# Optimization experiments

Hardware: AMD Instinct MI355X
Metric: run time of the kernel (lower is better)

Reference implementation:

```python
import jax, jax.numpy as jnp
import numpy as np

B, S, V, E, HL = 64, 30, 5000, 300, 256
TWOH = 2 * HL
KB, MAPD, MEMD, MLP, NCLS = 512, 512, 512, 1024, 32
L, T, NMOD, NOPS = 8, 9, 9, 6
IH, IW, CIN = 15, 10, 512 + 128


def setup_inputs():
    key = jax.random.key(0)
    ks = iter(jax.random.split(key, 64))
    g = lambda shape, s=0.05: jax.random.normal(next(ks), shape, jnp.float32) * s
    inp = {}
    inp['image'] = g((B, CIN, IH, IW), 1.0)
    inp['ques'] = jax.random.randint(next(ks), (B, S), 0, V)
    ql = jnp.sort(jax.random.randint(next(ks), (B,), 1, S + 1))[::-1]
    inp['q_len'] = ql.at[0].set(S)
    inp['embed_W'] = g((V, E))
    for d in ('f', 'b'):
        inp['lstm_Wi_' + d] = g((E, 4 * HL))
        inp['lstm_Wh_' + d] = g((HL, 4 * HL))
        inp['lstm_b_' + d] = jnp.zeros((4 * HL,), jnp.float32)
    inp['W1'] = g((T, TWOH, TWOH))
    inp['b_1'] = jnp.zeros((TWOH,), jnp.float32)
    inp['W2_w'] = g((2 * TWOH, TWOH)); inp['W2_b'] = jnp.zeros((TWOH,), jnp.float32)
    inp['W3'] = g((TWOH,))
    inp['c_0'] = g((TWOH,), 1.0)
    inp['Wmod'] = g((TWOH, NMOD))
    inp['ic1_w'] = g((KB, CIN)); inp['ic1_b'] = g((KB,), 1.0)
    inp['ic2_w'] = g((KB, KB)); inp['ic2_b'] = g((KB,), 1.0)
    inp['i2m_w'] = g((MAPD, KB)); inp['i2m_b'] = g((MAPD,), 1.0)
    inp['t2m_w'] = g((TWOH, MAPD)); inp['t2m_b'] = jnp.zeros((MAPD,), jnp.float32)
    inp['cell3_ow'] = g((4, NOPS), 1.0)
    inp['cell3_cw'] = g((4, MAPD)); inp['cell3_cb'] = jnp.zeros((4,), jnp.float32)
    inp['cell4_ow'] = g((2, NOPS), 1.0)
    inp['cell4_cw'] = g((2, MAPD)); inp['cell4_cb'] = jnp.zeros((2,), jnp.float32)
    inp['ans_ow'] = g((2, NOPS), 1.0)
    inp['ans_W'] = g((2, 2 * MAPD, MEMD)); inp['ans_b'] = jnp.zeros((2, MEMD), jnp.float32)
    inp['out1_w'] = g((TWOH + MEMD, MLP)); inp['out1_b'] = jnp.zeros((MLP,), jnp.float32)
    inp['out2_w'] = g((MLP, NCLS)); inp['out2_b'] = jnp.zeros((NCLS,), jnp.float32)
    return inp


def _conv1x1(x, w, b):
    return jnp.einsum('bchw,oc->bohw', x, w) + b[None, :, None, None]


def _lstm_dir(xW, Wh, mask, reverse):
    # xW: [S,B,4H], mask: [S,B,1] ; torch LSTM gate order i,f,g,o
    Bn, Hn = xW.shape[1], Wh.shape[0]
    def step(carry, inp):
        h, c = carry
        xw, m = inp
        z = xw + h @ Wh
        i, f, gg, o = jnp.split(z, 4, axis=-1)
        cn = jax.nn.sigmoid(f) * c + jax.nn.sigmoid(i) * jnp.tanh(gg)
        hn = jax.nn.sigmoid(o) * jnp.tanh(cn)
        return (jnp.where(m, hn, h), jnp.where(m, cn, c)), jnp.where(m, hn, 0.0)
    init = (jnp.zeros((Bn, Hn), xW.dtype), jnp.zeros((Bn, Hn), xW.dtype))
    (hF, _), outs = jax.lax.scan(step, init, (xW, mask), reverse=reverse)
    return hF, outs


def _mix3(ow, x, a, t):
    # soft op mixing (DARTS-style) for 3-input cells: x [B,D,H,W], a [B,H,W], t [B,D]
    w = jax.nn.softmax(ow)
    a4 = a[:, None]; t4 = t[:, :, None, None]
    ops = (x * t4, x + t4, x * a4, x * t4 * a4, x, a4 * t4)
    return jax.nn.elu(sum(w[k] * ops[k] for k in range(NOPS)))


def _mix4(ow, x, a1, a2, t):
    w = jax.nn.softmax(ow)
    a14 = a1[:, None]; a24 = a2[:, None]; t4 = t[:, :, None, None]
    ops = (x * t4, x + t4, x * a14, x * a24, x * a14 * a24, x * t4 * (a14 + a24))
    return jax.nn.elu(sum(w[k] * ops[k] for k in range(NOPS)))


def _forward(image, ques, q_len, embed_W, lstm_Wi_f, lstm_Wh_f, lstm_b_f, lstm_Wi_b, lstm_Wh_b, lstm_b_b, W1, b_1, W2_w, W2_b, W3, c_0, Wmod, ic1_w, ic1_b, ic2_w, ic2_b, i2m_w, i2m_b, t2m_w, t2m_b, cell3_ow, cell3_cw, cell3_cb, cell4_ow, cell4_cw, cell4_cb, ans_ow, ans_W, ans_b, out1_w, out1_b, out2_w, out2_b):
    # img_conv (1x1 conv -> ELU -> 1x1 conv)
    x = jax.nn.elu(_conv1x1(image, ic1_w, ic1_b))
    x = _conv1x1(x, ic2_w, ic2_b)
    Bn, _, Hh, Ww = x.shape
    Sn = ques.shape[1]
    # bi-LSTM over the (packed, i.e. masked) question
    emb = embed_W[ques]                                   # [B,S,E]
    mask = (jnp.arange(Sn)[None, :] < q_len[:, None])     # [B,S]
    mT = mask.T[:, :, None].astype(x.dtype) > 0           # [S,B,1] bool
    xWf = (emb @ lstm_Wi_f + lstm_b_f).transpose(1, 0, 2)
    xWb = (emb @ lstm_Wi_b + lstm_b_b).transpose(1, 0, 2)
    hF, oF = _lstm_dir(xWf, lstm_Wh_f, mT, False)
    hB, oB = _lstm_dir(xWb, lstm_Wh_b, mT, True)
    lstm_out = jnp.concatenate([oF, oB], -1).transpose(1, 0, 2)  # [B,S,2H], zero at pads
    q = jnp.concatenate([hF, hB], -1)                            # [B,2H]
    img_map = _conv1x1(x, i2m_w, i2m_b)                          # [B,MAP,H,W]
    stack = jnp.zeros((Bn, Hh, Ww, L), x.dtype)
    p = jnp.zeros((Bn, L), x.dtype).at[:, 0].set(1.0)
    mem = jnp.zeros((Bn, MEMD), x.dtype)
    c_prev = jnp.tile(c_0[None], (Bn, 1))
    e0 = jnp.zeros((L,), x.dtype).at[0].set(1.0)
    imp_loss = jnp.float32(0.0)
    read = lambda st, pp: jnp.einsum('bhwl,bl->bhw', st, pp)
    dec = lambda pp: jnp.concatenate([pp[:, 1:], jnp.zeros_like(pp[:, :1])], 1) + pp * e0
    for t in range(T):
        u = jnp.concatenate([q @ W1[t] + b_1, c_prev], 1) @ W2_w + W2_b  # [B,2H]
        wl = u @ Wmod                                                     # [B,9]
        ls = jax.nn.log_softmax(wl, axis=1)
        imp_loss = imp_loss - jnp.sum(jnp.exp(ls) * ls)
        w = jnp.exp(ls)
        attn = jax.nn.softmax(jnp.einsum('bsh,h->bs', lstm_out * u[:, None, :], W3), axis=1)
        c = jnp.einsum('bs,bsh->bh', attn, lstm_out)
        c_prev = c
        tmap = c @ t2m_w + t2m_b
        stacks, ps = [], []
        a_top = read(stack, p)     # attention at stack top
        # modules 0-3: overwrite at current pointer (pointer shift is commented out in source)
        for m in range(4):
            out = jnp.einsum('bdhw,d->bhw', _mix3(cell3_ow[m], img_map, a_top, tmap), cell3_cw[m]) + cell3_cb[m]
            pb = p[:, None, None, :]
            stacks.append(stack * (1.0 - pb) + out[..., None] * pb)
            ps.append(p)
        # modules 4-5: pop one (soft pointer decrement), then write
        p_dec = dec(p)
        a2 = read(stack, p_dec)
        for m in range(2):
            out = jnp.einsum('bdhw,d->bhw', _mix4(cell4_ow[m], img_map, a_top, a2, tmap), cell4_cw[m]) + cell4_cb[m]
            pb = p_dec[:, None, None, :]
            stacks.append(stack * (1.0 - pb) + out[..., None] * pb)
            ps.append(p_dec)
        # modules 6-7: answer cells -> memory update, stack untouched
        pooled6 = jnp.mean(_mix3(ans_ow[0], img_map, a_top, tmap), axis=(2, 3))
        mem6 = jnp.concatenate([pooled6, tmap], 1) @ ans_W[0] + ans_b[0]
        stacks.append(stack); ps.append(p)
        pooled7 = jnp.mean(_mix4(ans_ow[1], img_map, a_top, a2, tmap), axis=(2, 3))
        mem7 = jnp.concatenate([pooled7, tmap], 1) @ ans_W[1] + ans_b[1]
        stacks.append(stack); ps.append(p_dec)
        # module 8: NoOp
        stacks.append(stack); ps.append(p)
        # soft mixing over modules (the scatter-heavy part)
        stack = jnp.einsum('bm,bmhwl->bhwl', w, jnp.stack(stacks, 1))
        p = jnp.einsum('bm,bml->bl', w, jnp.stack(ps, 1))
        mem = w[:, 6:7] * mem6 + w[:, 7:8] * mem7 + (1.0 - w[:, 6:7] - w[:, 7:8]) * mem
    h1 = jax.nn.elu(jnp.concatenate([q, mem], 1) @ out1_w + out1_b)
    logits = h1 @ out2_w + out2_b
    return logits, imp_loss


def reference(image, ques, q_len, embed_W, lstm_Wi_f, lstm_Wh_f, lstm_b_f, lstm_Wi_b, lstm_Wh_b, lstm_b_b, W1, b_1, W2_w, W2_b, W3, c_0, Wmod, ic1_w, ic1_b, ic2_w, ic2_b, i2m_w, i2m_b, t2m_w, t2m_b, cell3_ow, cell3_cw, cell3_cb, cell4_ow, cell4_cw, cell4_cb, ans_ow, ans_W, ans_b, out1_w, out1_b, out2_w, out2_b):
    return _forward(image, ques, q_len, embed_W, lstm_Wi_f, lstm_Wh_f, lstm_b_f, lstm_Wi_b, lstm_Wh_b, lstm_b_b, W1, b_1, W2_w, W2_b, W3, c_0, Wmod, ic1_w, ic1_b, ic2_w, ic2_b, i2m_w, i2m_b, t2m_w, t2m_b, cell3_ow, cell3_cw, cell3_cb, cell4_ow, cell4_cw, cell4_cb, ans_ow, ans_W, ans_b, out1_w, out1_b, out2_w, out2_b)
```

## Files before the change

### kernel.cpp

```cpp
#include <hip/hip_runtime.h>
#include <math.h>

#define DEV __device__ __forceinline__

DEV float fexp(float x){ return __expf(x); }
DEV float elu_(float x){ return x > 0.f ? x : fexp(x) - 1.f; }
DEV float sigm_(float x){ return 1.f/(1.f + fexp(-x)); }
DEV float tanh_(float x){ float e = fexp(2.f*x); return 1.f - 2.f/(e + 1.f); }
DEV unsigned bf16r(float x){ unsigned u = __float_as_uint(x);
  return (u + 0x7fffu + ((u>>16)&1u)) >> 16; }
DEV float blo(unsigned u){ return __uint_as_float(u << 16); }
DEV float bhi(unsigned u){ return __uint_as_float(u & 0xffff0000u); }
DEV float bl(unsigned short u){ return __uint_as_float(((unsigned)u) << 16); }

using frag  = __attribute__((ext_vector_type(8))) short;
using f32x4 = __attribute__((ext_vector_type(4))) float;

DEV void d_pack4(const float* __restrict__ Whf, const float* __restrict__ Whb,
                 uint4* __restrict__ whp4, int idx)
{
  int dir = idx >> 15;
  int rem = idx & 32767;
  int kg  = rem >> 10;
  int n   = rem & 1023;
  const float* Wh = dir ? Whb : Whf;
  unsigned v[4];
#pragma unroll
  for (int j = 0; j < 4; ++j) {
    int k = kg*8 + 2*j;
    float lo = Wh[(size_t)k*1024 + n];
    float hi = Wh[(size_t)(k+1)*1024 + n];
    v[j] = bf16r(lo) | (bf16r(hi) << 16);
  }
  whp4[idx] = make_uint4(v[0], v[1], v[2], v[3]);
}

DEV void d_packB(const float* __restrict__ W, short* __restrict__ Bp,
                 int KC, int Ng, int Ksrc, int N, int trans, int idx)
{
  if (idx >= KC*Ng*64) return;
  int lane = idx & 63;
  int g    = (idx >> 6) % Ng;
  int kc   = idx / (64*Ng);
  int n = g*16 + (lane & 15);
  int kb = kc*32 + ((lane >> 4) << 3);
  unsigned o[4];
#pragma unroll
  for (int jj = 0; jj < 4; ++jj) {
    int k0 = kb + 2*jj;
    float v0 = (k0   < Ksrc) ? (trans ? W[(size_t)n*Ksrc + k0]   : W[(size_t)(k0)*N + n])   : 0.f;
    float v1 = (k0+1 < Ksrc) ? (trans ? W[(size_t)n*Ksrc + k0+1] : W[(size_t)(k0+1)*N + n]) : 0.f;
    o[jj] = bf16r(v0) | (bf16r(v1) << 16);
  }
  *(uint4*)(Bp + (size_t)idx*8) = make_uint4(o[0], o[1], o[2], o[3]);
}

DEV void d_packImg(const float* __restrict__ image, short* __restrict__ Ap, int idx)
{
  int lane = idx & 63;
  int kc   = (idx >> 6) % 20;
  int mt   = idx / 1280;
  int row = mt*16 + (lane & 15);
  int b = row / 150, p = row % 150;
  int cb = kc*32 + ((lane >> 4) << 3);
  unsigned o[4];
#pragma unroll
  for (int jj = 0; jj < 4; ++jj) {
    float v0 = image[((size_t)b*640 + cb + 2*jj    )*150 + p];
    float v1 = image[((size_t)b*640 + cb + 2*jj + 1)*150 + p];
    o[jj] = bf16r(v0) | (bf16r(v1) << 16);
  }
  *(uint4*)(Ap + (size_t)idx*8) = make_uint4(o[0], o[1], o[2], o[3]);
}

DEV void d_packEmb(const float* __restrict__ embedW, const int* __restrict__ ques,
                   short* __restrict__ Ap, int idx)
{
  int lane = idx & 63;
  int kc   = (idx >> 6) % 10;
  int mt   = idx / 640;
  int row = mt*16 + (lane & 15);
  int q = ques[row];
  int kb = kc*32 + ((lane >> 4) << 3);
  unsigned o[4];
#pragma unroll
  for (int jj = 0; jj < 4; ++jj) {
    int k0 = kb + 2*jj;
    float v0 = (k0   < 300) ? embedW[(size_t)q*300 + k0]   : 0.f;
    float v1 = (k0+1 < 300) ? embedW[(size_t)q*300 + k0+1] : 0.f;
    o[jj] = bf16r(v0) | (bf16r(v1) << 16);
  }
  *(uint4*)(Ap + (size_t)idx*8) = make_uint4(o[0], o[1], o[2], o[3]);
}

__global__ __launch_bounds__(256)
void megapack_k(const float* __restrict__ c0, const float* __restrict__ c3ow,
                const float* __restrict__ c4ow, const float* __restrict__ aow,
                float* __restrict__ stack, float* __restrict__ pvecA,
                float* __restrict__ mem, float* __restrict__ cprev,
                float* __restrict__ swb, float* __restrict__ pl,
                const float* __restrict__ Whf, const float* __restrict__ Whb,
                uint4* __restrict__ whp4,
                const float* __restrict__ ic1w, short* __restrict__ w1p,
                const float* __restrict__ ic2w, short* __restrict__ w2mp,
                const float* __restrict__ i2mw, short* __restrict__ w3mp,
                const float* __restrict__ Wif, short* __restrict__ wifp,
                const float* __restrict__ Wib, short* __restrict__ wibp,
                const float* __restrict__ image, short* __restrict__ imgP,
                const float* __restrict__ embedW, const int* __restrict__ ques,
                short* __restrict__ embp,
                const float* __restrict__ t2mw, unsigned* __restrict__ t2pp,
                const float* __restrict__ W2w, unsigned short* __restrict__ w2bp,
                const float* __restrict__ ansW, unsigned short* __restrict__ answp)
{
  const int bx = blockIdx.x, tid = threadIdx.x;
  if (bx < 320) {
    int idx = bx*256 + tid;
    int stride = 320*256;
    for (int i = idx; i < 64*150*8; i += stride) stack[i] = 0.f;
    for (int i = idx; i < 64*8;    i += stride) pvecA[i] = ((i & 7) == 0) ? 1.f : 0.f;
    for (int i = idx; i < 64*512;  i += stride) mem[i] = 0.f;
    for (int i = idx; i < 64*512;  i += stride) cprev[i] = c0[i & 511];
    for (int i = idx; i < 9*2*64*512; i += stride) pl[i] = 0.f;
    if (idx < 8) {
      const float* ow = (idx < 4) ? (c3ow + idx*6)
                      : (idx < 6) ? (c4ow + (idx-4)*6)
                                  : (aow  + (idx-6)*6);
      float mx = ow[0];
      for (int m = 1; m < 6; ++m) mx = fmaxf(mx, ow[m]);
      float e[6]; float s = 0.f;
      for (int m = 0; m < 6; ++m) { e[m] = fexp(ow[m]-mx); s += e[m]; }
      for (int m = 0; m < 6; ++m) swb[idx*6+m] = e[m]/s;
    }
  } else if (bx < 576) {
    d_pack4(Whf, Whb, whp4, (bx-320)*256 + tid);
  } else if (bx < 736) {
    d_packB(ic1w, w1p, 20, 32, 640, 512, 1, (bx-576)*256 + tid);
  } else if (bx < 864) {
    d_packB(ic2w, w2mp, 16, 32, 512, 512, 1, (bx-736)*256 + tid);
  } else if (bx < 992) {
    d_packB(i2mw, w3mp, 16, 32, 512, 512, 1, (bx-864)*256 + tid);
  } else if (bx < 1152) {
    d_packB(Wif, wifp, 10, 64, 300, 1024, 0, (bx-992)*256 + tid);
  } else if (bx < 1312) {
    d_packB(Wib, wibp, 10, 64, 300, 1024, 0, (bx-1152)*256 + tid);
  } else if (bx < 4312) {
    d_packImg(image, imgP, (bx-1312)*256 + tid);
  } else if (bx < 4612) {
    d_packEmb(embedW, ques, embp, (bx-4312)*256 + tid);
  } else if (bx < 5124) {
    int idx = (bx-4612)*256 + tid;
    int k = idx >> 8, c = idx & 255;
    t2pp[idx] = bf16r(t2mw[(size_t)k*512 + c]) | (bf16r(t2mw[(size_t)k*512 + 256 + c]) << 16);
  } else if (bx < 7172) {
    int i = (bx-5124)*256 + tid;
    w2bp[i] = (unsigned short)bf16r(W2w[i]);
  } else {
    int i = (bx-7172)*256 + tid;
    answp[i] = (unsigned short)bf16r(ansW[i]);
  }
}

__global__ __launch_bounds__(256)
void gemmM_k(const short* __restrict__ ApA, const short* __restrict__ ApB,
             const short* __restrict__ BpA, const short* __restrict__ BpB,
             const float* __restrict__ biasA, const float* __restrict__ biasB,
             void* __restrict__ CoutA, void* __restrict__ CoutB,
             int KC, int Ng, int N, int mode, int act, int KCout)
{
  __shared__ float lds[4][16][68];
  const int z = blockIdx.z;
  const short* Ap = z ? ApB : ApA;
  const short* Bp = z ? BpB : BpA;
  const float* bias = z ? biasB : biasA;
  void* Cout = z ? CoutB : CoutA;
  const int tid = threadIdx.x, lane = tid & 63, w = tid >> 6;
  const int mt = blockIdx.y*4 + w;
  const int ncol0 = blockIdx.x*64;
  const short* Abase = Ap + (((size_t)mt*KC) << 9) + lane*8;
  const short* Bbase = Bp + (((size_t)blockIdx.x*4) << 9) + lane*8;
  f32x4 acc0 = {0.f,0.f,0.f,0.f}, acc1 = acc0, acc2 = acc0, acc3 = acc0;
#pragma unroll 2
  for (int kc = 0; kc < KC; ++kc) {
    frag a = *(const frag*)(Abase + ((size_t)kc << 9));
    const short* bk = Bbase + (((size_t)kc*Ng) << 9);
    frag b0 = *(const frag*)(bk);
    frag b1 = *(const frag*)(bk + 512);
    frag b2 = *(const frag*)(bk + 1024);
    frag b3 = *(const frag*)(bk + 1536);
    acc0 = __builtin_amdgcn_mfma_f32_16x16x32_bf16(a, b0, acc0, 0, 0, 0);
    acc1 = __builtin_amdgcn_mfma_f32_16x16x32_bf16(a, b1, acc1, 0, 0, 0);
    acc2 = __builtin_amdgcn_mfma_f32_16x16x32_bf16(a, b2, acc2, 0, 0, 0);
    acc3 = __builtin_amdgcn_mfma_f32_16x16x32_bf16(a, b3, acc3, 0, 0, 0);
  }
  {
    int colb = lane & 15, rowb = (lane >> 4)*4;
#pragma unroll
    for (int r = 0; r < 4; ++r) {
      lds[w][rowb+r][ 0+colb] = acc0[r];
      lds[w][rowb+r][16+colb] = acc1[r];
      lds[w][rowb+r][32+colb] = acc2[r];
      lds[w][rowb+r][48+colb] = acc3[r];
    }
  }
  __syncthreads();
  if (mode == 0) {
    float* C = (float*)Cout;
    int mloc = lane >> 2, q4 = lane & 3;
    size_t rowoff = (size_t)(mt*16 + mloc)*N + ncol0 + q4*16;
#pragma unroll
    for (int i = 0; i < 4; ++i) {
      float4 v = *(float4*)&lds[w][mloc][q4*16 + i*4];
      const float* bp = bias + ncol0 + q4*16 + i*4;
      v.x += bp[0]; v.y += bp[1]; v.z += bp[2]; v.w += bp[3];
      if (act) { v.x = elu_(v.x); v.y = elu_(v.y); v.z = elu_(v.z); v.w = elu_(v.w); }
      *(float4*)&C[rowoff + i*4] = v;
    }
  } else if (mode == 1) {
    short* C = (short*)Cout;
    int m = lane & 15, qb = (lane >> 4)*8;
#pragma unroll
    for (int h = 0; h < 2; ++h) {
      int nl = h*32 + qb;
      unsigned o[4];
#pragma unroll
      for (int jj = 0; jj < 4; ++jj) {
        float v0 = lds[w][m][nl + 2*jj]     + bias[ncol0 + nl + 2*jj];
        float v1 = lds[w][m][nl + 2*jj + 1] + bias[ncol0 + nl + 2*jj + 1];
        if (act) { v0 = elu_(v0); v1 = elu_(v1); }
        o[jj] = bf16r(v0) | (bf16r(v1) << 16);
      }
      *(uint4*)(C + (((size_t)mt*KCout + (ncol0 >> 5) + h) << 9) + lane*8)
          = make_uint4(o[0], o[1], o[2], o[3]);
    }
  } else {
    unsigned short* C = (unsigned short*)Cout;
    int row = lane >> 2, cb = (lane & 3)*16;
#pragma unroll
    for (int h = 0; h < 2; ++h) {
      unsigned o[4];
#pragma unroll
      for (int jj = 0; jj < 4; ++jj) {
        float v0 = lds[w][row][cb + h*8 + 2*jj]     + bias[ncol0 + cb + h*8 + 2*jj];
        float v1 = lds[w][row][cb + h*8 + 2*jj + 1] + bias[ncol0 + cb + h*8 + 2*jj + 1];
        if (act) { v0 = elu_(v0); v1 = elu_(v1); }
        o[jj] = bf16r(v0) | (bf16r(v1) << 16);
      }
      *(uint4*)&C[(size_t)(mt*16 + row)*N + ncol0 + cb + h*8]
          = make_uint4(o[0], o[1], o[2], o[3]);
    }
  }
}

__global__ __launch_bounds__(512)
void gemm64b_k(const float* __restrict__ A1, long zA1, int K1log,
               const float* __restrict__ A2, int K2,
               const float* __restrict__ B, long zB,
               const float* __restrict__ bias, int zbias,
               float* __restrict__ C, long zC, int N, int act)
{
  const int K1 = 1 << K1log;
  const int Kt = K1 + K2;
  __shared__ __align__(16) float As[8][1024];
  __shared__ float part[8][8][64];
  const int tid = threadIdx.x;
  const int z = blockIdx.z;
  const int r0 = blockIdx.y*8;
  {
    const float* a1 = A1 + (size_t)z*zA1;
    const int nf4 = (8*K1) >> 2;
    for (int e4 = tid; e4 < nf4; e4 += 512) {
      int r = e4 >> (K1log-2);
      int k4 = (e4 & ((K1>>2)-1)) << 2;
      *(float4*)&As[r][k4] = *(const float4*)&a1[(size_t)(r0+r)*K1 + k4];
    }
    if (K2 > 0) {
      for (int e4 = tid; e4 < 1024; e4 += 512) {
        int r = e4 >> 7;
        int k4 = (e4 & 127) << 2;
        *(float4*)&As[r][K1+k4] = *(const float4*)&A2[(size_t)(r0+r)*512 + k4];
      }
    }
  }
  __syncthreads();
  const int lane = tid & 63, w = tid >> 6;
  const int n = blockIdx.x*64 + lane;
  const bool nv = n < N;
  const int kseg = Kt >> 3;
  const int k0 = w*kseg;
  const float* Bp = B + (size_t)z*zB + (size_t)k0*N + (nv ? n : 0);
  float acc[8] = {0,0,0,0,0,0,0,0};
#pragma unroll 8
  for (int kk = 0; kk < kseg; ++kk) {
    float bv = nv ? Bp[(size_t)kk*N] : 0.f;
    int k = k0 + kk;
#pragma unroll
    for (int r = 0; r < 8; ++r) acc[r] += As[r][k]*bv;
  }
#pragma unroll
  for (int r = 0; r < 8; ++r) part[w][r][lane] = acc[r];
  __syncthreads();
  {
    int r = tid >> 6, c = tid & 63;
    int nn = blockIdx.x*64 + c;
    if (nn < N) {
      float s = 0.f;
#pragma unroll
      for (int w2 = 0; w2 < 8; ++w2) s += part[w2][r][c];
      s += bias ? bias[(size_t)z*zbias + nn] : 0.f;
      if (act == 1) s = elu_(s);
      C[(size_t)z*zC + (size_t)(r0+r)*N + nn] = s;
    }
  }
}

__global__ __launch_bounds__(1024)
void lstm4_k(const float* __restrict__ xWf, const float* __restrict__ xWb,
             const uint4* __restrict__ whp4,
             const int* __restrict__ qlen, float* __restrict__ lstm_out,
             float* __restrict__ qout)
{
  int dir = blockIdx.x >> 6;
  int b   = blockIdx.x & 63;
  const float* xW = dir ? xWb : xWf;
  const uint4* Wp = whp4 + (size_t)dir*32768 + threadIdx.x;
  __shared__ __align__(16) float hl[256];
  __shared__ __align__(16) float cl[256];
  __shared__ float zl[1024];
  int tid = threadIdx.x;
  if (tid < 256) { hl[tid] = 0.f; cl[tid] = 0.f; }
  int len = qlen[b];
  for (int ss = 0; ss < 30; ++ss) {
    int s = dir ? (29-ss) : ss;
    __syncthreads();
    float z = xW[((size_t)b*30 + s)*1024 + tid];
#pragma unroll 4
    for (int kg = 0; kg < 32; ++kg) {
      uint4 w = Wp[(size_t)kg*1024];
      float4 ha = *(const float4*)&hl[kg*8];
      float4 hb = *(const float4*)&hl[kg*8+4];
      z += ha.x*blo(w.x) + ha.y*bhi(w.x) + ha.z*blo(w.y) + ha.w*bhi(w.y)
         + hb.x*blo(w.z) + hb.y*bhi(w.z) + hb.z*blo(w.w) + hb.w*bhi(w.w);
    }
    zl[tid] = z;
    __syncthreads();
    if (tid < 256) {
      float iv = zl[tid], fv = zl[256+tid], gv = zl[512+tid], ov = zl[768+tid];
      float cn = sigm_(fv)*cl[tid] + sigm_(iv)*tanh_(gv);
      float hn = sigm_(ov)*tanh_(cn);
      bool m = s < len;
      lstm_out[((size_t)b*30 + s)*512 + dir*256 + tid] = m ? hn : 0.f;
      if (m) { hl[tid] = hn; cl[tid] = cn; }
    }
  }
  __syncthreads();
  if (tid < 256) qout[(size_t)b*512 + dir*256 + tid] = hl[tid];
}

__global__ __launch_bounds__(1024)
void kcattn3_k(const float* __restrict__ u, const float* __restrict__ Wmod,
               const float* __restrict__ lstm_out, const float* __restrict__ W3,
               const unsigned* __restrict__ t2pp, const float* __restrict__ t2mb,
               float* __restrict__ woutAll, float* __restrict__ imp_part,
               float* __restrict__ cout, float* __restrict__ tmapv, int t)
{
  int b = blockIdx.x;
  int tid = threadIdx.x;
  int lane = tid & 63, wave = tid >> 6;
  __shared__ float ush[512];
  __shared__ float sC[512];
  __shared__ float cpart[512];
  __shared__ float tpart[4][512];
  __shared__ float wl[9];
  __shared__ float sc[32], at[32];
  if (tid < 512) ush[tid] = u[b*512 + tid];
  __syncthreads();
  for (int s = wave; s < 30; s += 16) {
    float acc = 0.f;
    const float* lo = lstm_out + ((size_t)b*30 + s)*512;
#pragma unroll
    for (int h = lane; h < 512; h += 64) acc += lo[h]*ush[h]*W3[h];
#pragma unroll
    for (int off = 32; off; off >>= 1) acc += __shfl_down(acc, off);
    if (lane == 0) sc[s] = acc;
  }
  if (wave < 9) {
    float acc = 0.f;
#pragma unroll
    for (int k = lane; k < 512; k += 64) acc += ush[k]*Wmod[k*9+wave];
#pragma unroll
    for (int off = 32; off; off >>= 1) acc += __shfl_down(acc, off);
    if (lane == 0) wl[wave] = acc;
  }
  __syncthreads();
  if (tid == 0) {
    float mx = wl[0];
    for (int m = 1; m < 9; ++m) mx = fmaxf(mx, wl[m]);
    float s = 0.f;
    for (int m = 0; m < 9; ++m) s += fexp(wl[m]-mx);
    float ls = logf(s);
    float ent = 0.f;
    for (int m = 0; m < 9; ++m) {
      float l = wl[m]-mx-ls;
      float w = fexp(l);
      woutAll[t*576 + b*9 + m] = w;
      ent -= w*l;
    }
    imp_part[t*64+b] = ent;
  }
  if (wave == 1) {
    float v = (lane < 30) ? sc[lane] : -3.4e38f;
    float mx = v;
#pragma unroll
    for (int off = 32; off; off >>= 1) mx = fmaxf(mx, __shfl_xor(mx, off));
    float e = (lane < 30) ? fexp(v-mx) : 0.f;
    float ssum = e;
#pragma unroll
    for (int off = 32; off; off >>= 1) ssum += __shfl_xor(ssum, off);
    if (lane < 30) at[lane] = e/ssum;
  }
  __syncthreads();
  {
    int h = tid & 511, seg = tid >> 9;
    float acc = 0.f;
    int s0 = seg ? 15 : 0, s1 = seg ? 30 : 15;
    for (int s = s0; s < s1; ++s) acc += at[s]*lstm_out[((size_t)b*30 + s)*512 + h];
    if (seg) cpart[h] = acc;
    __syncthreads();
    if (!seg) {
      float tot = acc + cpart[h];
      cout[b*512+h] = tot;
      sC[h] = tot;
    }
  }
  __syncthreads();
  {
    int c2 = tid & 255, ks = tid >> 8;
    float a0 = 0.f, a1 = 0.f;
    const unsigned* tp = t2pp + c2;
#pragma unroll 8
    for (int k = ks*128; k < ks*128 + 128; ++k) {
      float cv = sC[k];
      unsigned wv2 = tp[(size_t)k*256];
      a0 += cv*blo(wv2);
      a1 += cv*bhi(wv2);
    }
    tpart[ks][c2]       = a0;
    tpart[ks][256 + c2] = a1;
  }
  __syncthreads();
  if (tid < 512) {
    float v = tpart[0][tid] + tpart[1][tid] + tpart[2][tid] + tpart[3][tid];
    tmapv[b*512 + tid] = v + t2mb[tid];
  }
}

__global__ __launch_bounds__(256)
void modules2_k(const unsigned short* __restrict__ imapB, const float* __restrict__ tmapv,
                float* __restrict__ stack, const float* __restrict__ pvecIn,
                float* __restrict__ pvecOut,
                const float* __restrict__ swb, const float* __restrict__ c3w,
                const float* __restrict__ c3b, const float* __restrict__ c4w,
                const float* __restrict__ c4b, const float* __restrict__ wmod,
                float* __restrict__ plt)
{
  int b  = blockIdx.x;
  int pb = blockIdx.y;
  int lane = threadIdx.x & 63, wave = threadIdx.x >> 6;
  __shared__ float sT[512];
  __shared__ float pv[8], pd[8], wm[9];
  __shared__ float wpart[4][2][512];
  for (int j = threadIdx.x; j < 512; j += 256) sT[j] = tmapv[b*512 + j];
  if (threadIdx.x < 8) pv[threadIdx.x] = pvecIn[b*8+threadIdx.x];
  if (threadIdx.x >= 64 && threadIdx.x < 73) wm[threadIdx.x-64] = wmod[b*9 + threadIdx.x-64];
  __syncthreads();
  if (threadIdx.x < 8) {
    int l = threadIdx.x;
    pd[l] = (l < 7 ? pv[l+1] : 0.f) + (l == 0 ? pv[0] : 0.f);
  }
  __syncthreads();
  if (pb == 0 && threadIdx.x < 8) {
    int l = threadIdx.x;
    float WP = wm[0]+wm[1]+wm[2]+wm[3] + wm[6] + wm[8];
    float WD = wm[4]+wm[5] + wm[7];
    pvecOut[b*8+l] = WP*pv[l] + WD*pd[l];
  }

  float W[8][6];
#pragma unroll
  for (int m = 0; m < 8; ++m)
#pragma unroll
    for (int i = 0; i < 6; ++i) W[m][i] = swb[m*6+i];
  float W03 = wm[0]+wm[1]+wm[2]+wm[3];
  float W45 = wm[4]+wm[5];

  float acc6[8], acc7[8];
#pragma unroll
  for (int i = 0; i < 8; ++i) { acc6[i] = 0.f; acc7[i] = 0.f; }

  for (int pi = 0; pi < 2; ++pi) {
    int p = pb*8 + wave*2 + pi;
    if (p < 150) {
      const float* st = stack + ((size_t)b*150 + p)*8;
      float a = 0.f, av2 = 0.f;
#pragma unroll
      for (int l = 0; l < 8; ++l) { float v = st[l]; a += v*pv[l]; av2 += v*pd[l]; }
      float part[6] = {0,0,0,0,0,0};
#pragma unroll 2
      for (int i = 0; i < 8; ++i) {
        int d = i*64 + lane;
        float x = bl(imapB[((size_t)b*150 + p)*512 + d]);
        float t = sT[d];
#pragma unroll
        for (int m = 0; m < 4; ++m) {
          float c1 = W[m][0]*t + W[m][1] + W[m][4] + (W[m][2] + W[m][3]*t)*a;
          float c0 = W[m][1]*t + W[m][5]*t*a;
          part[m] += elu_(c1*x + c0) * c3w[m*512+d];
        }
#pragma unroll
        for (int m = 0; m < 2; ++m) {
          float c1 = W[4+m][0]*t + W[4+m][1] + W[4+m][2]*a + W[4+m][3]*av2
                   + W[4+m][4]*a*av2 + W[4+m][5]*t*(a+av2);
          part[4+m] += elu_(c1*x + W[4+m][1]*t) * c4w[m*512+d];
        }
        float c16 = W[6][0]*t + W[6][1] + W[6][4] + (W[6][2] + W[6][3]*t)*a;
        float c06 = W[6][1]*t + W[6][5]*t*a;
        acc6[i] += elu_(c16*x + c06);
        float c17 = W[7][0]*t + W[7][1] + W[7][2]*a + W[7][3]*av2
                  + W[7][4]*a*av2 + W[7][5]*t*(a+av2);
        acc7[i] += elu_(c17*x + W[7][1]*t);
      }
#pragma unroll
      for (int m = 0; m < 6; ++m) {
#pragma unroll
        for (int off = 32; off; off >>= 1) part[m] += __shfl_down(part[m], off);
        part[m] = __shfl(part[m], 0);
      }
      float r3  = wm[0]*(part[0]+c3b[0]) + wm[1]*(part[1]+c3b[1])
                + wm[2]*(part[2]+c3b[2]) + wm[3]*(part[3]+c3b[3]);
      float r45 = wm[4]*(part[4]+c4b[0]) + wm[5]*(part[5]+c4b[1]);
      if (lane < 8) {
        int l = lane;
        size_t idx = ((size_t)b*150 + p)*8 + l;
        stack[idx] = stack[idx]*(1.f - W03*pv[l] - W45*pd[l])
                   + pv[l]*r3 + pd[l]*r45;
      }
    }
  }
#pragma unroll
  for (int i = 0; i < 8; ++i) {
    wpart[wave][0][i*64+lane] = acc6[i];
    wpart[wave][1][i*64+lane] = acc7[i];
  }
  __syncthreads();
  for (int e = threadIdx.x; e < 1024; e += 256) {
    int which = e >> 9, d = e & 511;
    float s = wpart[0][which][d] + wpart[1][which][d]
            + wpart[2][which][d] + wpart[3][which][d];
    atomicAdd(&plt[(size_t)which*32768 + b*512 + d], s * (1.f/150.f));
  }
}

__global__ __launch_bounds__(512)
void ansu3_k(const float* __restrict__ plt, const float* __restrict__ tmapv,
             const unsigned short* __restrict__ answp, const float* __restrict__ ansb,
             float* __restrict__ m67o,
             const float* __restrict__ tmp1n, const float* __restrict__ cprev,
             const unsigned short* __restrict__ w2bp, const float* __restrict__ W2b,
             float* __restrict__ ubuf, int do_u)
{
  const int z = blockIdx.z;
  if (z == 2 && !do_u) return;
  __shared__ __align__(16) float As[8][1024];
  __shared__ float part[8][8][64];
  const int tid = threadIdx.x;
  const int r0 = blockIdx.y*8;
  const int nc0 = blockIdx.x*64;
  const int lane = tid & 63, w = tid >> 6;

  if (z < 2) {
    for (int e4 = tid; e4 < 1024; e4 += 512) {
      int r = e4 >> 7, k4 = (e4 & 127) << 2;
      *(float4*)&As[r][k4]     = *(const float4*)&plt[(size_t)z*32768 + (size_t)(r0+r)*512 + k4];
      *(float4*)&As[r][512+k4] = *(const float4*)&tmapv[(size_t)(r0+r)*512 + k4];
    }
  } else {
    for (int e4 = tid; e4 < 1024; e4 += 512) {
      int r = e4 >> 7, k4 = (e4 & 127) << 2;
      *(float4*)&As[r][k4]     = *(const float4*)&tmp1n[(size_t)(r0+r)*512 + k4];
      *(float4*)&As[r][512+k4] = *(const float4*)&cprev[(size_t)(r0+r)*512 + k4];
    }
  }
  __syncthreads();
  {
    const unsigned short* Bp = (z < 2 ? answp + (size_t)z*524288 : w2bp)
                             + (size_t)(w*128)*512 + nc0 + lane;
    float acc[8] = {0,0,0,0,0,0,0,0};
    int k0 = w*128;
#pragma unroll 8
    for (int kk = 0; kk < 128; ++kk) {
      float bv = bl(Bp[(size_t)kk*512]);
#pragma unroll
      for (int r = 0; r < 8; ++r) acc[r] += As[r][k0+kk]*bv;
    }
#pragma unroll
    for (int r = 0; r < 8; ++r) part[w][r][lane] = acc[r];
  }
  __syncthreads();
  {
    int r = tid >> 6, c = tid & 63;
    float s = 0.f;
#pragma unroll
    for (int w2 = 0; w2 < 8; ++w2) s += part[w2][r][c];
    if (z < 2) {
      m67o[((size_t)z*64 + r0 + r)*512 + nc0 + c] = s + ansb[z*512 + nc0 + c];
    } else {
      ubuf[(size_t)(r0+r)*512 + nc0 + c] = s + W2b[nc0 + c];
    }
  }
}

__global__ __launch_bounds__(512)
void memfin_k(const float* __restrict__ woutAll, const float* __restrict__ m67t,
              float* __restrict__ memb)
{
  int b = blockIdx.x;
  int tid = threadIdx.x;
  __shared__ float w6s[9], w7s[9], coef[9];
  if (tid < 9)       w6s[tid] = woutAll[tid*576 + b*9 + 6];
  else if (tid < 18) w7s[tid-9] = woutAll[(tid-9)*576 + b*9 + 7];
  __syncthreads();
  if (tid == 0) {
    float c = 1.f;
    for (int t = 8; t >= 0; --t) { coef[t] = c; c *= (1.f - w6s[t] - w7s[t]); }
  }
  __syncthreads();
  float acc = 0.f;
#pragma unroll
  for (int t = 0; t < 9; ++t) {
    float m6 = m67t[(((size_t)t*2 + 0)*64 + b)*512 + tid];
    float m7 = m67t[(((size_t)t*2 + 1)*64 + b)*512 + tid];
    acc += coef[t]*(w6s[t]*m6 + w7s[t]*m7);
  }
  memb[b*512 + tid] = acc;
}

__global__ __launch_bounds__(256)
void imp_k(const float* __restrict__ part, float* __restrict__ out)
{
  int lane = threadIdx.x & 63, wave = threadIdx.x >> 6;
  float acc = 0.f;
  for (int i = threadIdx.x; i < 576; i += 256) acc += part[i];
#pragma unroll
  for (int off = 32; off; off >>= 1) acc += __shfl_down(acc, off);
  __shared__ float red[4];
  if (lane == 0) red[wave] = acc;
  __syncthreads();
  if (threadIdx.x == 0) out[0] = red[0]+red[1]+red[2]+red[3];
}

extern "C" void kernel_launch(void* const* d_in, const int* in_sizes, int n_in,
                              void* d_out, int out_size, void* d_ws, size_t ws_size,
                              hipStream_t stream)
{
  (void)in_sizes; (void)n_in; (void)out_size; (void)ws_size;
  const float* image = (const float*)d_in[0];
  const int*   ques  = (const int*)d_in[1];
  const int*   qlen  = (const int*)d_in[2];
  const float* embedW= (const float*)d_in[3];
  const float* Wi_f  = (const float*)d_in[4];
  const float* Wh_f  = (const float*)d_in[5];
  const float* b_f   = (const float*)d_in[6];
  const float* Wi_b  = (const float*)d_in[7];
  const float* Wh_b  = (const float*)d_in[8];
  const float* b_b   = (const float*)d_in[9];
  const float* W1    = (const float*)d_in[10];
  const float* b1    = (const float*)d_in[11];
  const float* W2w   = (const float*)d_in[12];
  const float* W2b   = (const float*)d_in[13];
  const float* W3    = (const float*)d_in[14];
  const float* c0    = (const float*)d_in[15];
  const float* Wmod  = (const float*)d_in[16];
  const float* ic1w  = (const float*)d_in[17];
  const float* ic1b  = (const float*)d_in[18];
  const float* ic2w  = (const float*)d_in[19];
  const float* ic2b  = (const float*)d_in[20];
  const float* i2mw  = (const float*)d_in[21];
  const float* i2mb  = (const float*)d_in[22];
  const float* t2mw  = (const float*)d_in[23];
  const float* t2mb  = (const float*)d_in[24];
  const float* c3ow  = (const float*)d_in[25];
  const float* c3cw  = (const float*)d_in[26];
  const float* c3cb  = (const float*)d_in[27];
  const float* c4ow  = (const float*)d_in[28];
  const float* c4cw  = (const float*)d_in[29];
  const float* c4cb  = (const float*)d_in[30];
  const float* aow   = (const float*)d_in[31];
  const float* ansW  = (const float*)d_in[32];
  const float* ansb  = (const float*)d_in[33];
  const float* o1w   = (const float*)d_in[34];
  const float* o1b   = (const float*)d_in[35];
  const float* o2w   = (const float*)d_in[36];
  const float* o2b   = (const float*)d_in[37];
  float* out = (float*)d_out;
  float* ws  = (float*)d_ws;

  size_t off = 0;
  auto alloc = [&](size_t n){ float* p = ws + off; off += n; return p; };
  short* imgP  = (short*)alloc(600ull*20*64*8/2);
  short* X1p   = (short*)alloc(600ull*16*64*8/2);
  short* X2p   = (short*)alloc(600ull*16*64*8/2);
  short* w1p   = (short*)alloc(20*32*64*8/2);
  short* w2mp  = (short*)alloc(16*32*64*8/2);
  short* w3mp  = (short*)alloc(16*32*64*8/2);
  short* wifp  = (short*)alloc(10*64*64*8/2);
  short* wibp  = (short*)alloc(10*64*64*8/2);
  short* embp  = (short*)alloc(120ull*10*64*8/2);
  unsigned short* imapB = (unsigned short*)alloc(9600ull*512/2);
  unsigned* t2pp = (unsigned*)alloc(512*256);
  unsigned short* w2bp  = (unsigned short*)alloc(524288/2);
  unsigned short* answp = (unsigned short*)alloc(1048576/2);
  float* xWfb  = alloc(64ull*30*1024);
  float* xWbb  = alloc(64ull*30*1024);
  float* lout  = alloc(64ull*30*512);
  float* qbuf  = alloc(64*512);
  float* stck  = alloc(64*150*8);
  float* pvecA = alloc(64*8);
  float* pvecB = alloc(64*8);
  float* memb  = alloc(64*512);
  float* cprev = alloc(64*512);
  float* tmp1a = alloc(9ull*64*512);
  float* ubuf  = alloc(64*512);
  float* wmwA  = alloc(9*64*9);
  float* impp  = alloc(9*64);
  float* swb   = alloc(48);
  float* pl    = alloc(9ull*2*64*512);
  float* m67t  = alloc(9ull*2*64*512);
  float* tmapv = alloc(64*512);
  float* h1b   = alloc(64*1024);
  uint4* whp4  = (uint4*)alloc(2*32*1024*4);

  megapack_k<<<11268, 256, 0, stream>>>(
      c0, c3ow, c4ow, aow, stck, pvecA, memb, cprev, swb, pl,
      Wh_f, Wh_b, whp4,
      ic1w, w1p, ic2w, w2mp, i2mw, w3mp, Wi_f, wifp, Wi_b, wibp,
      image, imgP, embedW, ques, embp, t2mw, t2pp,
      W2w, w2bp, ansW, answp);

  gemmM_k<<<dim3(8,150,1), 256, 0, stream>>>(imgP, imgP, w1p, w1p, ic1b, ic1b,
                                             X1p, X1p, 20, 32, 512, 1, 1, 16);
  gemmM_k<<<dim3(8,150,1), 256, 0, stream>>>(X1p, X1p, w2mp, w2mp, ic2b, ic2b,
                                             X2p, X2p, 16, 32, 512, 1, 0, 16);
  gemmM_k<<<dim3(8,150,1), 256, 0, stream>>>(X2p, X2p, w3mp, w3mp, i2mb, i2mb,
                                             imapB, imapB, 16, 32, 512, 2, 0, 0);
  gemmM_k<<<dim3(16,30,2), 256, 0, stream>>>(embp, embp, wifp, wibp, b_f, b_b,
                                             xWfb, xWbb, 10, 64, 1024, 0, 0, 0);

  lstm4_k<<<128, 1024, 0, stream>>>(xWfb, xWbb, whp4, qlen, lout, qbuf);

  gemm64b_k<<<dim3(8,8,9), 512, 0, stream>>>(
      qbuf, 0, 9, (const float*)nullptr, 0,
      W1, 262144, b1, 0, tmp1a, 32768, 512, 0);
  gemm64b_k<<<dim3(8,8,1), 512, 0, stream>>>(
      tmp1a, 0, 9, cprev, 512, W2w, 0, W2b, 0, ubuf, 0, 512, 0);

  for (int t = 0; t < 9; ++t) {
    float* pvIn  = (t & 1) ? pvecB : pvecA;
    float* pvOut = (t & 1) ? pvecA : pvecB;
    kcattn3_k<<<64, 1024, 0, stream>>>(ubuf, Wmod, lout, W3, t2pp, t2mb,
                                       wmwA, impp, cprev, tmapv, t);
    modules2_k<<<dim3(64,19), 256, 0, stream>>>(
        imapB, tmapv, stck, pvIn, pvOut, swb, c3cw, c3cb, c4cw, c4cb,
        wmwA + (size_t)t*576, pl + (size_t)t*65536);
    ansu3_k<<<dim3(8,8,3), 512, 0, stream>>>(
        pl + (size_t)t*65536, tmapv, answp, ansb, m67t + (size_t)t*65536,
        tmp1a + (size_t)(t < 8 ? t+1 : 0)*32768, cprev, w2bp, W2b, ubuf,
        (t < 8) ? 1 : 0);
  }

  memfin_k<<<64, 512, 0, stream>>>(wmwA, m67t, memb);
  gemm64b_k<<<dim3(16,8,1), 512, 0, stream>>>(
      qbuf, 0, 9, memb, 512, o1w, 0, o1b, 0, h1b, 0, 1024, 1);
  gemm64b_k<<<dim3(1,8,1), 512, 0, stream>>>(
      h1b, 0, 10, (const float*)nullptr, 0, o2w, 0, o2b, 0, out, 0, 32, 0);
  imp_k<<<1, 256, 0, stream>>>(impp, out + 2048);
}
```

Measured before the change: 909.0 us.

## Rewrite LSTM recurrence as MFMA fp16 kernel with cross-block flag sync

```diff
diff --git a/kernel.cpp b/kernel.cpp
--- a/kernel.cpp
+++ b/kernel.cpp
@@ -1,4 +1,5 @@
 #include <hip/hip_runtime.h>
+#include <hip/hip_fp16.h>
 #include <math.h>
 
 #define DEV __device__ __forceinline__
@@ -14,26 +15,8 @@
 DEV float bl(unsigned short u){ return __uint_as_float(((unsigned)u) << 16); }
 
 using frag  = __attribute__((ext_vector_type(8))) short;
+using fragh = __attribute__((ext_vector_type(8))) _Float16;
 using f32x4 = __attribute__((ext_vector_type(4))) float;
-
-DEV void d_pack4(const float* __restrict__ Whf, const float* __restrict__ Whb,
-                 uint4* __restrict__ whp4, int idx)
-{
-  int dir = idx >> 15;
-  int rem = idx & 32767;
-  int kg  = rem >> 10;
-  int n   = rem & 1023;
-  const float* Wh = dir ? Whb : Whf;
-  unsigned v[4];
-#pragma unroll
-  for (int j = 0; j < 4; ++j) {
-    int k = kg*8 + 2*j;
-    float lo = Wh[(size_t)k*1024 + n];
-    float hi = Wh[(size_t)(k+1)*1024 + n];
-    v[j] = bf16r(lo) | (bf16r(hi) << 16);
-  }
-  whp4[idx] = make_uint4(v[0], v[1], v[2], v[3]);
-}
 
 DEV void d_packB(const float* __restrict__ W, short* __restrict__ Bp,
                  int KC, int Ng, int Ksrc, int N, int trans, int idx)
@@ -100,7 +83,8 @@
                 float* __restrict__ mem, float* __restrict__ cprev,
                 float* __restrict__ swb, float* __restrict__ pl,
                 const float* __restrict__ Whf, const float* __restrict__ Whb,
-                uint4* __restrict__ whp4,
+                unsigned* __restrict__ whT,
+                float* __restrict__ hbufz, int* __restrict__ flagz,
                 const float* __restrict__ ic1w, short* __restrict__ w1p,
                 const float* __restrict__ ic2w, short* __restrict__ w2mp,
                 const float* __restrict__ i2mw, short* __restrict__ w3mp,
@@ -122,6 +106,8 @@
     for (int i = idx; i < 64*512;  i += stride) mem[i] = 0.f;
     for (int i = idx; i < 64*512;  i += stride) cprev[i] = c0[i & 511];
     for (int i = idx; i < 9*2*64*512; i += stride) pl[i] = 0.f;
+    for (int i = idx; i < 32768;   i += stride) hbufz[i] = 0.f;
+    if (idx < 256) flagz[idx] = 0;
     if (idx < 8) {
       const float* ow = (idx < 4) ? (c3ow + idx*6)
                       : (idx < 6) ? (c4ow + (idx-4)*6)
@@ -132,31 +118,39 @@
       for (int m = 0; m < 6; ++m) { e[m] = fexp(ow[m]-mx); s += e[m]; }
       for (int m = 0; m < 6; ++m) swb[idx*6+m] = e[m]/s;
     }
-  } else if (bx < 576) {
-    d_pack4(Whf, Whb, whp4, (bx-320)*256 + tid);
-  } else if (bx < 736) {
-    d_packB(ic1w, w1p, 20, 32, 640, 512, 1, (bx-576)*256 + tid);
-  } else if (bx < 864) {
-    d_packB(ic2w, w2mp, 16, 32, 512, 512, 1, (bx-736)*256 + tid);
-  } else if (bx < 992) {
-    d_packB(i2mw, w3mp, 16, 32, 512, 512, 1, (bx-864)*256 + tid);
-  } else if (bx < 1152) {
-    d_packB(Wif, wifp, 10, 64, 300, 1024, 0, (bx-992)*256 + tid);
-  } else if (bx < 1312) {
-    d_packB(Wib, wibp, 10, 64, 300, 1024, 0, (bx-1152)*256 + tid);
-  } else if (bx < 4312) {
-    d_packImg(image, imgP, (bx-1312)*256 + tid);
-  } else if (bx < 4612) {
-    d_packEmb(embedW, ques, embp, (bx-4312)*256 + tid);
-  } else if (bx < 5124) {
-    int idx = (bx-4612)*256 + tid;
+  } else if (bx < 1344) {
+    int idx = (bx-320)*256 + tid;
+    int dd  = idx >> 17;
+    int rem = idx & 131071;
+    int kp  = rem >> 10;
+    int zc  = rem & 1023;
+    const float* Wh = dd ? Whb : Whf;
+    __half2 hv = __floats2half2_rn(Wh[(size_t)(2*kp)*1024 + zc],
+                                   Wh[(size_t)(2*kp+1)*1024 + zc]);
+    whT[((size_t)dd << 17) + (zc << 7) + kp] = *(unsigned*)&hv;
+  } else if (bx < 1504) {
+    d_packB(ic1w, w1p, 20, 32, 640, 512, 1, (bx-1344)*256 + tid);
+  } else if (bx < 1632) {
+    d_packB(ic2w, w2mp, 16, 32, 512, 512, 1, (bx-1504)*256 + tid);
+  } else if (bx < 1760) {
+    d_packB(i2mw, w3mp, 16, 32, 512, 512, 1, (bx-1632)*256 + tid);
+  } else if (bx < 1920) {
+    d_packB(Wif, wifp, 10, 64, 300, 1024, 0, (bx-1760)*256 + tid);
+  } else if (bx < 2080) {
+    d_packB(Wib, wibp, 10, 64, 300, 1024, 0, (bx-1920)*256 + tid);
+  } else if (bx < 5080) {
+    d_packImg(image, imgP, (bx-2080)*256 + tid);
+  } else if (bx < 5380) {
+    d_packEmb(embedW, ques, embp, (bx-5080)*256 + tid);
+  } else if (bx < 5892) {
+    int idx = (bx-5380)*256 + tid;
     int k = idx >> 8, c = idx & 255;
     t2pp[idx] = bf16r(t2mw[(size_t)k*512 + c]) | (bf16r(t2mw[(size_t)k*512 + 256 + c]) << 16);
-  } else if (bx < 7172) {
-    int i = (bx-5124)*256 + tid;
+  } else if (bx < 7940) {
+    int i = (bx-5892)*256 + tid;
     w2bp[i] = (unsigned short)bf16r(W2w[i]);
   } else {
-    int i = (bx-7172)*256 + tid;
+    int i = (bx-7940)*256 + tid;
     answp[i] = (unsigned short)bf16r(ansW[i]);
   }
 }
@@ -314,47 +308,95 @@
   }
 }
 
-__global__ __launch_bounds__(1024)
-void lstm4_k(const float* __restrict__ xWf, const float* __restrict__ xWb,
-             const uint4* __restrict__ whp4,
-             const int* __restrict__ qlen, float* __restrict__ lstm_out,
-             float* __restrict__ qout)
-{
-  int dir = blockIdx.x >> 6;
-  int b   = blockIdx.x & 63;
-  const float* xW = dir ? xWb : xWf;
-  const uint4* Wp = whp4 + (size_t)dir*32768 + threadIdx.x;
-  __shared__ __align__(16) float hl[256];
-  __shared__ __align__(16) float cl[256];
-  __shared__ float zl[1024];
-  int tid = threadIdx.x;
-  if (tid < 256) { hl[tid] = 0.f; cl[tid] = 0.f; }
-  int len = qlen[b];
+__global__ __launch_bounds__(256)
+void lstmM_k(const float* __restrict__ xWf, const float* __restrict__ xWb,
+             const unsigned* __restrict__ whT, const int* __restrict__ qlen,
+             unsigned short* __restrict__ hbuf, int* __restrict__ flags,
+             float* __restrict__ lstm_out, float* __restrict__ qout)
+{
+  const int bx = blockIdx.x;
+  const int d = bx & 1, g = (bx >> 1) & 3, n = bx >> 3;
+  const int tid = threadIdx.x, lane = tid & 63, w = tid >> 6;
+  const int q = lane >> 4, cl = lane & 15;
+  __shared__ __align__(16) unsigned short Wl[65536];
+
+#pragma unroll 4
+  for (int rb = 0; rb < 32; ++rb) {
+    int lcrow = rb*8 + (tid >> 5);
+    int gt = lcrow >> 6, c = lcrow & 63;
+    int zc = gt*256 + n*64 + c;
+    uint4 v = *(const uint4*)(whT + (((size_t)d*1024 + zc) << 7) + ((tid & 31) << 2));
+    int byteoff = (lcrow << 9) + ((((tid & 31) << 4)) ^ ((lcrow & 7) << 4));
+    *(uint4*)((char*)Wl + byteoff) = v;
+  }
+
+  const float* xW = d ? xWb : xWf;
+  const int hc = n*64 + w*16 + cl;
+  const int b0 = g*16 + q*4;
+  const int len0 = qlen[b0], len1 = qlen[b0+1], len2 = qlen[b0+2], len3 = qlen[b0+3];
+  f32x4 cst = {0.f,0.f,0.f,0.f}, hst = cst;
+  int* flg = flags + ((d*4 + g) << 5);
+  const int bofs = (cl & 7) << 4;
+  __syncthreads();
+
   for (int ss = 0; ss < 30; ++ss) {
-    int s = dir ? (29-ss) : ss;
+    const int s = d ? (29 - ss) : ss;
+    float xw0[4], xw1[4], xw2[4], xw3[4];
+#pragma unroll
+    for (int r = 0; r < 4; ++r) {
+      const float* xr = xW + (size_t)(b0 + r)*30720 + (size_t)s*1024 + hc;
+      xw0[r] = xr[0]; xw1[r] = xr[256]; xw2[r] = xr[512]; xw3[r] = xr[768];
+    }
+    if (ss > 0) {
+      if (tid == 0) {
+        while (__hip_atomic_load(&flg[ss-1], __ATOMIC_RELAXED,
+                                 __HIP_MEMORY_SCOPE_AGENT) < 4)
+          __builtin_amdgcn_s_sleep(1);
+      }
+      __syncthreads();
+      __threadfence();
+    }
+    const unsigned short* hbr = hbuf + ((size_t)(((ss & 1)*2 + d)*4 + g) << 12);
+    f32x4 acc0 = {0.f,0.f,0.f,0.f}, acc1 = acc0, acc2 = acc0, acc3 = acc0;
+#pragma unroll
+    for (int ks = 0; ks < 8; ++ks) {
+      fragh a = *(const fragh*)((const char*)hbr + (cl << 9) + (ks << 6) + (q << 4));
+      const int kb = ((ks << 6) + (q << 4)) ^ bofs;
+      const char* wb = (const char*)Wl + ((w*16 + cl) << 9) + kb;
+      fragh bf0 = *(const fragh*)(wb);
+      fragh bf1 = *(const fragh*)(wb + (64 << 9));
+      fragh bf2 = *(const fragh*)(wb + (128 << 9));
+      fragh bf3 = *(const fragh*)(wb + (192 << 9));
+      acc0 = __builtin_amdgcn_mfma_f32_16x16x32_f16(a, bf0, acc0, 0, 0, 0);
+      acc1 = __builtin_amdgcn_mfma_f32_16x16x32_f16(a, bf1, acc1, 0, 0, 0);
+      acc2 = __builtin_amdgcn_mfma_f32_16x16x32_f16(a, bf2, acc2, 0, 0, 0);
+      acc3 = __builtin_amdgcn_mfma_f32_16x16x32_f16(a, bf3, acc3, 0, 0, 0);
+    }
+    unsigned short* hbw = hbuf + ((size_t)((((ss & 1) ^ 1)*2 + d)*4 + g) << 12);
+#pragma unroll
+    for (int r = 0; r < 4; ++r) {
+      const int b = b0 + r;
+      float iv = acc0[r] + xw0[r];
+      float fv = acc1[r] + xw1[r];
+      float gv = acc2[r] + xw2[r];
+      float ov = acc3[r] + xw3[r];
+      float cn = sigm_(fv)*cst[r] + sigm_(iv)*tanh_(gv);
+      float hn = sigm_(ov)*tanh_(cn);
+      const int len = (r==0) ? len0 : (r==1) ? len1 : (r==2) ? len2 : len3;
+      const bool m = s < len;
+      float hk = m ? hn : hst[r];
+      cst[r] = m ? cn : cst[r];
+      hst[r] = hk;
+      lstm_out[(((size_t)b*30 + s) << 9) + (d << 8) + hc] = m ? hn : 0.f;
+      hbw[(q*4 + r)*256 + hc] = __half_as_ushort(__float2half(hk));
+    }
+    __threadfence();
     __syncthreads();
-    float z = xW[((size_t)b*30 + s)*1024 + tid];
-#pragma unroll 4
-    for (int kg = 0; kg < 32; ++kg) {
-      uint4 w = Wp[(size_t)kg*1024];
-      float4 ha = *(const float4*)&hl[kg*8];
-      float4 hb = *(const float4*)&hl[kg*8+4];
-      z += ha.x*blo(w.x) + ha.y*bhi(w.x) + ha.z*blo(w.y) + ha.w*bhi(w.y)
-         + hb.x*blo(w.z) + hb.y*bhi(w.z) + hb.z*blo(w.w) + hb.w*bhi(w.w);
-    }
-    zl[tid] = z;
-    __syncthreads();
-    if (tid < 256) {
-      float iv = zl[tid], fv = zl[256+tid], gv = zl[512+tid], ov = zl[768+tid];
-      float cn = sigm_(fv)*cl[tid] + sigm_(iv)*tanh_(gv);
-      float hn = sigm_(ov)*tanh_(cn);
-      bool m = s < len;
-      lstm_out[((size_t)b*30 + s)*512 + dir*256 + tid] = m ? hn : 0.f;
-      if (m) { hl[tid] = hn; cl[tid] = cn; }
-    }
-  }
-  __syncthreads();
-  if (tid < 256) qout[(size_t)b*512 + dir*256 + tid] = hl[tid];
+    if (tid == 0) atomicAdd(&flg[ss], 1);
+  }
+#pragma unroll
+  for (int r = 0; r < 4; ++r)
+    qout[((size_t)(b0 + r) << 9) + (d << 8) + hc] = hst[r];
 }
 
 __global__ __launch_bounds__(1024)
@@ -738,11 +780,13 @@
   float* m67t  = alloc(9ull*2*64*512);
   float* tmapv = alloc(64*512);
   float* h1b   = alloc(64*1024);
-  uint4* whp4  = (uint4*)alloc(2*32*1024*4);
-
-  megapack_k<<<11268, 256, 0, stream>>>(
+  unsigned* whT = (unsigned*)alloc(2ull*1024*128);
+  float* hbufW  = alloc(32768);
+  int*   flagsI = (int*)alloc(256);
+
+  megapack_k<<<12036, 256, 0, stream>>>(
       c0, c3ow, c4ow, aow, stck, pvecA, memb, cprev, swb, pl,
-      Wh_f, Wh_b, whp4,
+      Wh_f, Wh_b, whT, hbufW, flagsI,
       ic1w, w1p, ic2w, w2mp, i2mw, w3mp, Wi_f, wifp, Wi_b, wibp,
       image, imgP, embedW, ques, embp, t2mw, t2pp,
       W2w, w2bp, ansW, answp);
@@ -756,7 +800,8 @@
   gemmM_k<<<dim3(16,30,2), 256, 0, stream>>>(embp, embp, wifp, wibp, b_f, b_b,
                                              xWfb, xWbb, 10, 64, 1024, 0, 0, 0);
 
-  lstm4_k<<<128, 1024, 0, stream>>>(xWfb, xWbb, whp4, qlen, lout, qbuf);
+  lstmM_k<<<32, 256, 0, stream>>>(xWfb, xWbb, whT, qlen,
+                                  (unsigned short*)hbufW, flagsI, lout, qbuf);
 
   gemm64b_k<<<dim3(8,8,9), 512, 0, stream>>>(
       qbuf, 0, 9, (const float*)nullptr, 0,
```

Measured after the change: 980.8 us. +7.9%, slower.
